# Kernel optimization log

Measured on AMD Instinct MI355X. Metric: run time of the kernel, lower is better.

Reference implementation:

```python
import jax, jax.numpy as jnp
import numpy as np


def _lstm_layer(x, Wih, Whh, b):
    # torch nn.LSTM single layer, batch_first, gates in i,f,g,o order
    B, T, _ = x.shape
    H = Whh.shape[1]
    xg = jnp.einsum('btd,gd->btg', x, Wih) + b  # precompute input gates (B,T,4H)

    def step(carry, g_t):
        h, c = carry
        g = g_t + h @ Whh.T
        i, f, gg, o = jnp.split(g, 4, axis=-1)
        c = jax.nn.sigmoid(f) * c + jax.nn.sigmoid(i) * jnp.tanh(gg)
        h = jax.nn.sigmoid(o) * jnp.tanh(c)
        return (h, c), h

    z = jnp.zeros((B, H), x.dtype)
    _, hs = jax.lax.scan(step, (z, z), jnp.swapaxes(xg, 0, 1))
    return jnp.swapaxes(hs, 0, 1)


def _forward(x, x_lens, word_starts, word_ends, word_lens, tail_frames,
             fW_ih0, fW_hh0, fb0, fW_ih1, fW_hh1, fb1, fW_ih2, fW_hh2, fb2,
             fpW, fpb, wpW, wpb, lnW, lnB, wW_ih, wW_hh, wb, spW, spb):
    B, T, _ = x.shape
    # 3-layer frame LSTM (eval mode: inter-layer dropout disabled)
    h = _lstm_layer(x, fW_ih0, fW_hh0, fb0)
    h = _lstm_layer(h, fW_ih1, fW_hh1, fb1)
    h = _lstm_layer(h, fW_ih2, fW_hh2, fb2)
    # pad_packed_sequence zeros outputs beyond each sequence length
    tmask = (jnp.arange(T)[None, :] < x_lens[:, None]).astype(h.dtype)
    h = h * tmask[..., None]
    y_frame = h @ fpW.T + fpb  # (B,T,srv)

    # ragged per-word tail mean: r_j = mean h[i0:ef], i0 = max(ef-tail, sf)
    W = word_ends.shape[1]
    ef = jnp.minimum(word_ends, x_lens[:, None])
    sf = jnp.maximum(word_starts, 0)
    i0 = jnp.maximum(ef - tail_frames, sf)
    valid = ((jnp.arange(W)[None, :] < word_lens[:, None]) & (word_ends > 0)
             & (ef > sf) & (ef > i0))
    t = jnp.arange(T)
    m = (valid[:, :, None] & (t[None, None, :] >= i0[:, :, None])
         & (t[None, None, :] < ef[:, :, None])).astype(h.dtype)  # (B,W,T)
    cnt = jnp.maximum(m.sum(-1), 1.0)
    reps = jnp.einsum('bwt,bth->bwh', m, h) / cnt[..., None]  # (B,W,FH)

    # word_proj: Linear + LayerNorm + GELU (eval: dropout/noise/word-dropout off)
    r = reps @ wpW.T + wpb
    mu = r.mean(-1, keepdims=True)
    var = ((r - mu) ** 2).mean(-1, keepdims=True)
    r = (r - mu) / jnp.sqrt(var + 1e-5) * lnW + lnB
    r = jax.nn.gelu(r, approximate=False)

    lens = jnp.maximum(word_lens, 1)
    c = _lstm_layer(r, wW_ih, wW_hh, wb)
    wmask = (jnp.arange(W)[None, :] < lens[:, None]).astype(c.dtype)
    c = c * wmask[..., None]  # pad_packed(total_length=W) zeros
    pred_sem = c @ spW.T + spb  # (B,W,srv)
    return y_frame, x_lens, pred_sem


def setup_inputs() -> dict:
    key = jax.random.key(0)
    ks = jax.random.split(key, 24)
    B, T, D, SRV, FH, WR, WH, W = 16, 2000, 80, 512, 512, 256, 256, 100
    x = jax.random.normal(ks[0], (B, T, D), jnp.float32)
    x_lens = jax.random.randint(ks[1], (B,), T // 2, T + 1).at[0].set(T)
    ends = jnp.sort(jax.random.randint(ks[2], (B, W), 1, T + 1), axis=1)
    starts = jnp.concatenate([jnp.zeros((B, 1), ends.dtype), ends[:, :-1]], axis=1)
    word_lens = jax.random.randint(ks[3], (B,), 1, W + 1)

    def u(k, shape, fan):
        s = 1.0 / np.sqrt(fan)
        return jax.random.uniform(k, shape, jnp.float32, -s, s)

    return {
        'x': x, 'x_lens': x_lens, 'word_starts': starts, 'word_ends': ends,
        'word_lens': word_lens, 'tail_frames': 10,
        'fW_ih0': u(ks[4], (4 * FH, D), FH), 'fW_hh0': u(ks[5], (4 * FH, FH), FH), 'fb0': u(ks[6], (4 * FH,), FH),
        'fW_ih1': u(ks[7], (4 * FH, FH), FH), 'fW_hh1': u(ks[8], (4 * FH, FH), FH), 'fb1': u(ks[9], (4 * FH,), FH),
        'fW_ih2': u(ks[10], (4 * FH, FH), FH), 'fW_hh2': u(ks[11], (4 * FH, FH), FH), 'fb2': u(ks[12], (4 * FH,), FH),
        'fpW': u(ks[13], (SRV, FH), FH), 'fpb': u(ks[14], (SRV,), FH),
        'wpW': u(ks[15], (WR, FH), FH), 'wpb': u(ks[16], (WR,), FH),
        'lnW': jnp.ones((WR,), jnp.float32), 'lnB': jnp.zeros((WR,), jnp.float32),
        'wW_ih': u(ks[17], (4 * WH, WR), WH), 'wW_hh': u(ks[18], (4 * WH, WH), WH), 'wb': u(ks[19], (4 * WH,), WH),
        'spW': u(ks[20], (SRV, WH), WH), 'spb': u(ks[21], (SRV,), WH),
    }


def reference(x, x_lens, word_starts, word_ends, word_lens, tail_frames,
              fW_ih0, fW_hh0, fb0, fW_ih1, fW_hh1, fb1, fW_ih2, fW_hh2, fb2,
              fpW, fpb, wpW, wpb, lnW, lnB, wW_ih, wW_hh, wb, spW, spb):
    return _forward(x, x_lens, word_starts, word_ends, word_lens, tail_frames,
                    fW_ih0, fW_hh0, fb0, fW_ih1, fW_hh1, fb1, fW_ih2, fW_hh2, fb2,
                    fpW, fpb, wpW, wpb, lnW, lnB, wW_ih, wW_hh, wb, spW, spb)
```

## Files before the change

kernel.cpp:

```cpp
#include <hip/hip_runtime.h>
#include <math.h>

typedef unsigned short u16;
typedef unsigned int   u32;
typedef unsigned long long u64;
typedef __attribute__((ext_vector_type(8))) short short8;
typedef __attribute__((ext_vector_type(4))) float f32x4;

__device__ __forceinline__ float bf2f(u16 v) { return __uint_as_float(((u32)v) << 16); }
__device__ __forceinline__ u16 f2bf(float f) {
    u32 u = __float_as_uint(f);
    u32 r = (u + 0x7fffu + ((u >> 16) & 1u)) >> 16;
    return (u16)r;
}
__device__ __forceinline__ u32 pk2(float a, float b) {
    return ((u32)f2bf(a)) | (((u32)f2bf(b)) << 16);
}
__device__ __forceinline__ float sigm(float x) { return 1.f / (1.f + __expf(-x)); }
__device__ __forceinline__ f32x4 mfma16(short8 a, short8 b, f32x4 c) {
    return __builtin_amdgcn_mfma_f32_16x16x32_bf16(a, b, c, 0, 0, 0);
}
__device__ __forceinline__ short8 ld8bf(const float* p) {
    short8 r;
#pragma unroll
    for (int j = 0; j < 8; ++j) r[j] = (short)f2bf(p[j]);
    return r;
}
__device__ __forceinline__ short8 ldg16cv(const u16* p) {
    short8 r;
    asm volatile("global_load_dwordx4 %0, %1, off sc0 sc1" : "=v"(r) : "v"(p));
    return r;
}
__device__ __forceinline__ void waitvm() {
    asm volatile("s_waitcnt vmcnt(0)" ::: "memory");
}

#define FLAG_STRIDE 16
#define NPAR 8
#define BIGF (1 << 26)
#define XL_OFF 16384000
#define PS_OFF 16384016

#define WS_FLAGS   0
#define WS_HBUF_F  32768
#define WS_HBUF_W  425984
#define WS_REPS    491520
#define WS_RW      3768320
#define WS_HSEQ    4587520
#define WS_FPWB    6225920

template<int KTIN, bool L0>
__device__ __forceinline__ void frame_body(
    const int layer, const int kwg,
    const float* __restrict__ Wih, const float* __restrict__ Whh, const float* __restrict__ bias,
    const float* __restrict__ x, u16* __restrict__ hbuf, int* __restrict__ flags,
    float* __restrict__ h3out, float* sC, float* scs, u16* sxpad, u16* AsIn, u16* AsOwn)
{
    const int tid  = threadIdx.x;
    const int lane = tid & 63;
    const int wave = tid >> 6;
    const int n16  = lane & 15;
    const int quad = lane >> 4;
    const int koff = quad * 8;

    for (int e = tid; e < 144; e += 128) scs[e] = 0.f;
    if (L0) {
        for (int e = tid; e < 256; e += 128) sxpad[(e >> 4) * 96 + 80 + (e & 15)] = 0;
    }

    const int grow = wave * 1024 + ((n16 >> 3) * 512) + kwg * 8 + (n16 & 7);
    short8 bfr[KTIN + 16];
#pragma unroll
    for (int kt = 0; kt < KTIN; ++kt) {
        short8 v = {0,0,0,0,0,0,0,0};
        const int k = kt * 32 + koff;
        if (L0) { if (k + 8 <= 80) v = ld8bf(Wih + grow * 80 + k); }
        else    { v = ld8bf(Wih + (size_t)grow * 512 + k); }
        bfr[kt] = v;
    }
#pragma unroll
    for (int kt = 0; kt < 16; ++kt)
        bfr[KTIN + kt] = ld8bf(Whh + (size_t)grow * 512 + kt * 32 + koff);

    const int pb = (tid >> 4) & 3;
    const int cb = kwg * 8 + pb * 2;
    const float bI0 = bias[cb],        bI1 = bias[cb + 1];
    const float bF0 = bias[512 + cb],  bF1 = bias[512 + cb + 1];
    const float bG0 = bias[1024 + cb], bG1 = bias[1024 + cb + 1];
    const float bO0 = bias[1536 + cb], bO1 = bias[1536 + cb + 1];

    const int* fP = flags + (layer * 64) * FLAG_STRIDE;
    const int* fO = flags + ((layer + 1) * 64) * FLAG_STRIDE;
    const int* fN = flags + ((layer + 2) * 64) * FLAG_STRIDE;
    int* myflag   = flags + ((layer + 1) * 64 + kwg) * FLAG_STRIDE;
    __syncthreads();

    for (int t = 0; t < 2000; ++t) {
        if (wave == 0) {
            int guard = 0;
            for (;;) {
                const int fp = __hip_atomic_load(fP + lane * FLAG_STRIDE, __ATOMIC_RELAXED, __HIP_MEMORY_SCOPE_AGENT);
                const int fo = __hip_atomic_load(fO + lane * FLAG_STRIDE, __ATOMIC_RELAXED, __HIP_MEMORY_SCOPE_AGENT);
                const int fn = __hip_atomic_load(fN + lane * FLAG_STRIDE, __ATOMIC_RELAXED, __HIP_MEMORY_SCOPE_AGENT);
                if (__all((fp >= t + 1) && (fo >= t) && (fn >= t - 7))) break;
                if (++guard > (1 << 22)) break;
                __builtin_amdgcn_s_sleep(1);
            }
        }
        __syncthreads();

        const u16* hown = hbuf + ((size_t)(layer * NPAR + ((t + 7) & 7))) * 8192;
        short8 rin[8], rown[8];
        float4 xv0, xv1, xv2;
        if (L0) {
            const int e0 = tid, e1 = tid + 128, e2 = tid + 256;
            xv0 = *(const float4*)(x + ((size_t)(e0 / 20) * 2000 + t) * 80 + (e0 % 20) * 4);
            xv1 = *(const float4*)(x + ((size_t)(e1 / 20) * 2000 + t) * 80 + (e1 % 20) * 4);
            if (e2 < 320)
                xv2 = *(const float4*)(x + ((size_t)(e2 / 20) * 2000 + t) * 80 + (e2 % 20) * 4);
        } else {
            const u16* hin = hbuf + ((size_t)((layer - 1) * NPAR + (t & 7))) * 8192;
#pragma unroll
            for (int i = 0; i < 8; ++i) rin[i] = ldg16cv(hin + (tid + 128 * i) * 8);
        }
#pragma unroll
        for (int i = 0; i < 8; ++i) rown[i] = ldg16cv(hown + (tid + 128 * i) * 8);
        waitvm();
        if (L0) {
            const int e0 = tid, e1 = tid + 128, e2 = tid + 256;
            u32* d0 = (u32*)(sxpad + (e0 / 20) * 96 + (e0 % 20) * 4);
            d0[0] = pk2(xv0.x, xv0.y); d0[1] = pk2(xv0.z, xv0.w);
            u32* d1 = (u32*)(sxpad + (e1 / 20) * 96 + (e1 % 20) * 4);
            d1[0] = pk2(xv1.x, xv1.y); d1[1] = pk2(xv1.z, xv1.w);
            if (e2 < 320) {
                u32* d2 = (u32*)(sxpad + (e2 / 20) * 96 + (e2 % 20) * 4);
                d2[0] = pk2(xv2.x, xv2.y); d2[1] = pk2(xv2.z, xv2.w);
            }
        }
#pragma unroll
        for (int i = 0; i < 8; ++i) {
            const int c = tid + 128 * i;
            const int row = c >> 6, col8 = (c & 63) << 3;
            if (!L0) *(short8*)(AsIn + row * 520 + col8) = rin[i];
            *(short8*)(AsOwn + row * 520 + col8) = rown[i];
        }
        __syncthreads();

        f32x4 acc[4] = {{0,0,0,0},{0,0,0,0},{0,0,0,0},{0,0,0,0}};
#pragma unroll
        for (int kt = 0; kt < KTIN; ++kt) {
            short8 a;
            if (L0) a = *(const short8*)(sxpad + n16 * 96 + kt * 32 + koff);
            else    a = *(const short8*)(AsIn + n16 * 520 + kt * 32 + koff);
            acc[kt & 3] = mfma16(a, bfr[kt], acc[kt & 3]);
        }
#pragma unroll
        for (int kt = 0; kt < 16; ++kt) {
            short8 a = *(const short8*)(AsOwn + n16 * 520 + kt * 32 + koff);
            acc[(KTIN + kt) & 3] = mfma16(a, bfr[KTIN + kt], acc[(KTIN + kt) & 3]);
        }
        const f32x4 C = acc[0] + acc[1] + acc[2] + acc[3];
#pragma unroll
        for (int r = 0; r < 4; ++r)
            sC[(wave * 16 + quad * 4 + r) * 17 + n16] = C[r];
        __syncthreads();

        if (tid < 64) {
            const int b = tid & 15, p = tid >> 4;
            u32 pk = 0;
#pragma unroll
            for (int e = 0; e < 2; ++e) {
                const int jl = p * 2 + e;
                const float gi = sC[b * 17 + jl]             + (e ? bI1 : bI0);
                const float gf = sC[b * 17 + 8 + jl]         + (e ? bF1 : bF0);
                const float gg = sC[(16 + b) * 17 + jl]      + (e ? bG1 : bG0);
                const float go = sC[(16 + b) * 17 + 8 + jl]  + (e ? bO1 : bO0);
                const float cp = scs[b * 9 + jl];
                const float cn = sigm(gf) * cp + sigm(gi) * tanhf(gg);
                const float hn = sigm(go) * tanhf(cn);
                scs[b * 9 + jl] = cn;
                pk |= ((u32)f2bf(hn)) << (16 * e);
                if (!L0 && layer == 2)
                    h3out[((size_t)(b * 2000 + t)) * 512 + kwg * 8 + p * 2 + e] = hn;
            }
            u32* hdst = (u32*)(hbuf + ((size_t)(layer * NPAR + (t & 7))) * 8192 + b * 512 + kwg * 8 + p * 2);
            __hip_atomic_store(hdst, pk, __ATOMIC_RELAXED, __HIP_MEMORY_SCOPE_AGENT);
            waitvm();
            if (tid == 0)
                __hip_atomic_store(myflag, t + 1, __ATOMIC_RELAXED, __HIP_MEMORY_SCOPE_AGENT);
        }
    }
}

__global__ __launch_bounds__(128, 1) void k_frame_lstm(
    const float* __restrict__ x,
    const float* __restrict__ Wih0, const float* __restrict__ Whh0, const float* __restrict__ b0,
    const float* __restrict__ Wih1, const float* __restrict__ Whh1, const float* __restrict__ b1,
    const float* __restrict__ Wih2, const float* __restrict__ Whh2, const float* __restrict__ b2,
    u16* hbuf, int* flags, float* h3out)
{
    __shared__ __align__(16) u16 sxpad[16 * 96];
    __shared__ __align__(16) u16 AsIn[16 * 520];
    __shared__ __align__(16) u16 AsOwn[16 * 520];
    __shared__ float sC[32 * 17];
    __shared__ float scs[16 * 9];
    const int wgid = blockIdx.x;
    const int layer = wgid >> 6;
    const int kwg = wgid & 63;
    if (layer == 0)      frame_body<3,  true >(0, kwg, Wih0, Whh0, b0, x, hbuf, flags, h3out, sC, scs, sxpad, AsIn, AsOwn);
    else if (layer == 1) frame_body<16, false>(1, kwg, Wih1, Whh1, b1, x, hbuf, flags, h3out, sC, scs, sxpad, AsIn, AsOwn);
    else                 frame_body<16, false>(2, kwg, Wih2, Whh2, b2, x, hbuf, flags, h3out, sC, scs, sxpad, AsIn, AsOwn);
}

__global__ __launch_bounds__(128, 1) void k_word_lstm(
    const u16* __restrict__ rW, const float* __restrict__ Wih,
    const float* __restrict__ Whh, const float* __restrict__ bias,
    u16* __restrict__ hbufw, int* __restrict__ flags, float* __restrict__ hseq)
{
    __shared__ float sC[32 * 17];
    __shared__ float scs[16 * 9];
    const int tid = threadIdx.x;
    const int lane = tid & 63;
    const int wave = tid >> 6;
    const int n16 = lane & 15;
    const int quad = lane >> 4;
    const int koff = quad * 8;
    const int kwg = blockIdx.x;

    for (int e = tid; e < 144; e += 128) scs[e] = 0.f;
    const int grow = wave * 512 + ((n16 >> 3) * 256) + kwg * 8 + (n16 & 7);
    short8 bfr[16];
#pragma unroll
    for (int kt = 0; kt < 8; ++kt) bfr[kt]     = ld8bf(Wih + (size_t)grow * 256 + kt * 32 + koff);
#pragma unroll
    for (int kt = 0; kt < 8; ++kt) bfr[8 + kt] = ld8bf(Whh + (size_t)grow * 256 + kt * 32 + koff);
    const int pb = (tid >> 4) & 3;
    const int cb = kwg * 8 + pb * 2;
    const float bI0 = bias[cb],       bI1 = bias[cb + 1];
    const float bF0 = bias[256 + cb], bF1 = bias[256 + cb + 1];
    const float bG0 = bias[512 + cb], bG1 = bias[512 + cb + 1];
    const float bO0 = bias[768 + cb], bO1 = bias[768 + cb + 1];
    const int* fO = flags + 320 * FLAG_STRIDE;
    int* myflag   = flags + (320 + kwg) * FLAG_STRIDE;
    __syncthreads();
    const int aoff = n16 * 256 + koff;

    for (int t = 0; t < 100; ++t) {
        if (wave == 0) {
            int guard = 0;
            for (;;) {
                const int fo = (lane < 32)
                    ? __hip_atomic_load(fO + lane * FLAG_STRIDE, __ATOMIC_RELAXED, __HIP_MEMORY_SCOPE_AGENT)
                    : BIGF;
                if (__all(fo >= t)) break;
                if (++guard > (1 << 22)) break;
                __builtin_amdgcn_s_sleep(1);
            }
        }
        __syncthreads();
        const u16* hown = hbufw + ((size_t)((t + 7) & 7)) * 4096;
        short8 ha[8];
#pragma unroll
        for (int kt = 0; kt < 8; ++kt) ha[kt] = ldg16cv(hown + aoff + kt * 32);
        f32x4 acc[4] = {{0,0,0,0},{0,0,0,0},{0,0,0,0},{0,0,0,0}};
#pragma unroll
        for (int kt = 0; kt < 8; ++kt) {
            short8 a = *(const short8*)(rW + ((size_t)(n16 * 100 + t)) * 256 + koff + kt * 32);
            acc[kt & 3] = mfma16(a, bfr[kt], acc[kt & 3]);
        }
        waitvm();
#pragma unroll
        for (int kt = 0; kt < 8; ++kt)
            acc[kt & 3] = mfma16(ha[kt], bfr[8 + kt], acc[kt & 3]);
        const f32x4 C = acc[0] + acc[1] + acc[2] + acc[3];
#pragma unroll
        for (int r = 0; r < 4; ++r) sC[(wave * 16 + quad * 4 + r) * 17 + n16] = C[r];
        __syncthreads();
        if (tid < 64) {
            const int b = tid & 15, p = tid >> 4;
            u32 pk = 0;
#pragma unroll
            for (int e = 0; e < 2; ++e) {
                const int jl = p * 2 + e;
                const float gi = sC[b * 17 + jl]            + (e ? bI1 : bI0);
                const float gf = sC[b * 17 + 8 + jl]        + (e ? bF1 : bF0);
                const float gg = sC[(16 + b) * 17 + jl]     + (e ? bG1 : bG0);
                const float go = sC[(16 + b) * 17 + 8 + jl] + (e ? bO1 : bO0);
                const float cp = scs[b * 9 + jl];
                const float cn = sigm(gf) * cp + sigm(gi) * tanhf(gg);
                const float hn = sigm(go) * tanhf(cn);
                scs[b * 9 + jl] = cn;
                pk |= ((u32)f2bf(hn)) << (16 * e);
                hseq[((size_t)(b * 100 + t)) * 256 + kwg * 8 + p * 2 + e] = hn;
            }
            u32* hdst = (u32*)(hbufw + ((size_t)(t & 7)) * 4096 + b * 256 + kwg * 8 + p * 2);
            __hip_atomic_store(hdst, pk, __ATOMIC_RELAXED, __HIP_MEMORY_SCOPE_AGENT);
            waitvm();
            if (tid == 0)
                __hip_atomic_store(myflag, t + 1, __ATOMIC_RELAXED, __HIP_MEMORY_SCOPE_AGENT);
        }
    }
}

__global__ void k_pool(const float* __restrict__ h3, const int* __restrict__ x_lens,
                       const int* __restrict__ wstarts, const int* __restrict__ wends,
                       const int* __restrict__ wlens, const int* __restrict__ tailp,
                       float* __restrict__ reps)
{
    const int rw = blockIdx.x;
    const int b = rw / 100, w = rw - b * 100;
    const int tid = threadIdx.x;
    const int xl = x_lens[b];
    const int we = wends[rw];
    const int s0 = wstarts[rw];
    const int wl = wlens[b];
    const int tail = tailp[0];
    int ef = we < xl ? we : xl;
    int sf = s0 > 0 ? s0 : 0;
    int i0 = ef - tail; if (i0 < sf) i0 = sf;
    const bool valid = (w < wl) && (we > 0) && (ef > sf) && (ef > i0);
    float a0 = 0.f, a1 = 0.f;
    if (valid) {
        for (int t = i0; t < ef; ++t) {
            const float* hp = h3 + ((size_t)(b * 2000 + t)) * 512;
            a0 += hp[tid];
            a1 += hp[tid + 256];
        }
        const float inv = 1.f / (float)(ef - i0);
        a0 *= inv; a1 *= inv;
    }
    reps[(size_t)rw * 512 + tid] = a0;
    reps[(size_t)rw * 512 + tid + 256] = a1;
}

__global__ __launch_bounds__(256, 2) void k_frame_proj(
    float* __restrict__ y, const int* __restrict__ x_lens,
    const u16* __restrict__ fpWb, const float* __restrict__ fpb)
{
    __shared__ __align__(16) u16 As[16 * 520];
    const int tid = threadIdx.x, lane = tid & 63, wave = tid >> 6;
    const int n16 = lane & 15, quad = lane >> 4, koff = quad * 8;
    const int blk = blockIdx.x;
    const int b = blk / 125;
    const int t0 = (blk - b * 125) * 16;
    const int xl = x_lens[b];
    for (int c = tid; c < 2048; c += 256) {
        const int row = c >> 7;
        const int q = c & 127;
        const int t = t0 + row;
        float4 v = {0.f, 0.f, 0.f, 0.f};
        if (t < xl) v = *(const float4*)(y + ((size_t)(b * 2000 + t)) * 512 + q * 4);
        u32* d = (u32*)(As + row * 520 + q * 4);
        d[0] = pk2(v.x, v.y);
        d[1] = pk2(v.z, v.w);
    }
    __syncthreads();
    const size_t rowbase = (size_t)b * 2000 + t0;
    for (int ct = 0; ct < 8; ++ct) {
        const int col0 = (wave * 8 + ct) * 16;
        f32x4 acc = {0, 0, 0, 0};
#pragma unroll
        for (int kt = 0; kt < 16; ++kt) {
            short8 a = *(const short8*)(As + n16 * 520 + kt * 32 + koff);
            short8 wv = *(const short8*)(fpWb + ((size_t)(col0 + n16)) * 512 + kt * 32 + koff);
            acc = mfma16(a, wv, acc);
        }
        const float bn = fpb[col0 + n16];
#pragma unroll
        for (int r = 0; r < 4; ++r) {
            const int m = quad * 4 + r;
            y[(rowbase + m) * 512 + col0 + n16] = acc[r] + bn;
        }
    }
}

__global__ void k_word_proj(const float* __restrict__ reps, const float* __restrict__ wpW,
                            const float* __restrict__ wpb, const float* __restrict__ lnW,
                            const float* __restrict__ lnB, u16* __restrict__ rW)
{
    __shared__ float sx[512];
    __shared__ float red[512];
    const int tid = threadIdx.x;
    const int row = blockIdx.x;
    for (int k = tid; k < 512; k += 256) sx[k] = reps[(size_t)row * 512 + k];
    __syncthreads();
    float acc = wpb[tid];
    const float4* wr = (const float4*)(wpW + (size_t)tid * 512);
    for (int k4 = 0; k4 < 128; ++k4) {
        const float4 w = wr[k4];
        acc += sx[k4 * 4] * w.x + sx[k4 * 4 + 1] * w.y + sx[k4 * 4 + 2] * w.z + sx[k4 * 4 + 3] * w.w;
    }
    red[tid] = acc; red[256 + tid] = acc * acc;
    __syncthreads();
    for (int s = 128; s > 0; s >>= 1) {
        if (tid < s) { red[tid] += red[tid + s]; red[256 + tid] += red[256 + tid + s]; }
        __syncthreads();
    }
    const float mu = red[0] * (1.f / 256.f);
    float var = red[256] * (1.f / 256.f) - mu * mu;
    if (var < 0.f) var = 0.f;
    const float xn = (acc - mu) * rsqrtf(var + 1e-5f);
    const float yv = xn * lnW[tid] + lnB[tid];
    const float g = 0.5f * yv * (1.0f + erff(yv * 0.70710678118654752f));
    rW[(size_t)row * 256 + tid] = f2bf(g);
}

__global__ void k_pred(const float* __restrict__ hseq, const int* __restrict__ wlens,
                       const float* __restrict__ spW, const float* __restrict__ spb,
                       float* __restrict__ out)
{
    __shared__ float sh[256];
    const int tid = threadIdx.x;
    const int rw = blockIdx.x;
    const int b = rw / 100, w = rw - b * 100;
    int wl = wlens[b]; if (wl < 1) wl = 1;
    const bool valid = (w < wl);
    sh[tid] = valid ? hseq[(size_t)rw * 256 + tid] : 0.f;
    __syncthreads();
    for (int o = tid; o < 512; o += 256) {
        float acc = spb[o];
        const float4* wr = (const float4*)(spW + (size_t)o * 256);
        for (int k4 = 0; k4 < 64; ++k4) {
            const float4 wv = wr[k4];
            acc += sh[k4 * 4] * wv.x + sh[k4 * 4 + 1] * wv.y + sh[k4 * 4 + 2] * wv.z + sh[k4 * 4 + 3] * wv.w;
        }
        out[PS_OFF + (size_t)rw * 512 + o] = acc;
    }
}

__global__ void k_xlens(const int* __restrict__ x_lens, float* __restrict__ out)
{
    const int tid = threadIdx.x;
    if (tid < 16) out[XL_OFF + tid] = (float)x_lens[tid];
}

__global__ void k_cvt(const float* __restrict__ src, u16* __restrict__ dst)
{
    const int e = blockIdx.x * 256 + threadIdx.x;
    const float4 v = *(const float4*)(src + (size_t)e * 4);
    u32* d = (u32*)(dst + (size_t)e * 4);
    d[0] = pk2(v.x, v.y);
    d[1] = pk2(v.z, v.w);
}

__global__ void k_init(u32* __restrict__ p)
{
    const int idx = blockIdx.x * 256 + threadIdx.x;
    u32 v = 0u;
    if (idx < 8192) {
        const int slot = idx >> 4;
        if (slot < 64 || (slot >= 256 && slot < 320)) v = (u32)BIGF;
    }
    p[idx] = v;
}

extern "C" void kernel_launch(void* const* d_in, const int* in_sizes, int n_in,
                              void* d_out, int out_size, void* d_ws, size_t ws_size,
                              hipStream_t stream)
{
    (void)in_sizes; (void)n_in; (void)out_size; (void)ws_size;
    const float* x    = (const float*)d_in[0];
    const int* x_lens = (const int*)d_in[1];
    const int* wstart = (const int*)d_in[2];
    const int* wend   = (const int*)d_in[3];
    const int* wlen   = (const int*)d_in[4];
    const int* tailp  = (const int*)d_in[5];
    const float* Wih0 = (const float*)d_in[6];
    const float* Whh0 = (const float*)d_in[7];
    const float* b0   = (const float*)d_in[8];
    const float* Wih1 = (const float*)d_in[9];
    const float* Whh1 = (const float*)d_in[10];
    const float* b1   = (const float*)d_in[11];
    const float* Wih2 = (const float*)d_in[12];
    const float* Whh2 = (const float*)d_in[13];
    const float* b2   = (const float*)d_in[14];
    const float* fpW  = (const float*)d_in[15];
    const float* fpb  = (const float*)d_in[16];
    const float* wpW  = (const float*)d_in[17];
    const float* wpb  = (const float*)d_in[18];
    const float* lnW  = (const float*)d_in[19];
    const float* lnB  = (const float*)d_in[20];
    const float* wWih = (const float*)d_in[21];
    const float* wWhh = (const float*)d_in[22];
    const float* wb   = (const float*)d_in[23];
    const float* spW  = (const float*)d_in[24];
    const float* spb  = (const float*)d_in[25];

    float* out = (float*)d_out;
    char* ws = (char*)d_ws;
    int* flags  = (int*)(ws + WS_FLAGS);
    u16* hbufF  = (u16*)(ws + WS_HBUF_F);
    u16* hbufW  = (u16*)(ws + WS_HBUF_W);
    float* reps = (float*)(ws + WS_REPS);
    u16* rW     = (u16*)(ws + WS_RW);
    float* hseq = (float*)(ws + WS_HSEQ);
    u16* fpWb   = (u16*)(ws + WS_FPWB);

    k_init<<<480, 256, 0, stream>>>((u32*)d_ws);
    k_cvt<<<256, 256, 0, stream>>>(fpW, fpWb);
    k_frame_lstm<<<192, 128, 0, stream>>>(x, Wih0, Whh0, b0, Wih1, Whh1, b1,
                                          Wih2, Whh2, b2, hbufF, flags, out);
    k_pool<<<1600, 256, 0, stream>>>(out, x_lens, wstart, wend, wlen, tailp, reps);
    k_frame_proj<<<2000, 256, 0, stream>>>(out, x_lens, fpWb, fpb);
    k_word_proj<<<1600, 256, 0, stream>>>(reps, wpW, wpb, lnW, lnB, rW);
    k_word_lstm<<<32, 128, 0, stream>>>(rW, wWih, wWhh, wb, hbufW, flags, hseq);
    k_pred<<<1600, 256, 0, stream>>>(hseq, wlen, spW, spb, out);
    k_xlens<<<1, 64, 0, stream>>>(x_lens, out);
}
```

Before: 7.718 ms.

## Replace per-step flag polling with self-validating bit-inverted hidden-state buffers

Hidden states are now stored bit-inverted, so a zero word means "not yet written". Consumers spin directly on the data until every word is nonzero, which replaces the per-step polling of producer flags. The ring buffer grows to 16 slots, and each workgroup zeroes a slot ahead of use. Only the next layer's progress flag is still checked, which removes a flag round-trip and a barrier from the serial recurrence. The gate nonlinearity now runs on all 128 threads instead of 64, with the cell state kept in registers. The cost is a correctness dependency on the zero-sentinel encoding and on memory ordering between the clearing stores and later writes.

```diff
diff --git a/kernel.cpp b/kernel.cpp
--- a/kernel.cpp
+++ b/kernel.cpp
@@ -6,8 +6,8 @@
 typedef unsigned long long u64;
 typedef __attribute__((ext_vector_type(8))) short short8;
 typedef __attribute__((ext_vector_type(4))) float f32x4;
-
-__device__ __forceinline__ float bf2f(u16 v) { return __uint_as_float(((u32)v) << 16); }
+typedef __attribute__((ext_vector_type(4))) unsigned int u32x4;
+
 __device__ __forceinline__ u16 f2bf(float f) {
     u32 u = __float_as_uint(f);
     u32 r = (u + 0x7fffu + ((u >> 16) & 1u)) >> 16;
@@ -26,35 +26,41 @@
     for (int j = 0; j < 8; ++j) r[j] = (short)f2bf(p[j]);
     return r;
 }
-__device__ __forceinline__ short8 ldg16cv(const u16* p) {
-    short8 r;
+__device__ __forceinline__ u32x4 ldg16cv4(const u16* p) {
+    u32x4 r;
     asm volatile("global_load_dwordx4 %0, %1, off sc0 sc1" : "=v"(r) : "v"(p));
     return r;
 }
 __device__ __forceinline__ void waitvm() {
     asm volatile("s_waitcnt vmcnt(0)" ::: "memory");
 }
+__device__ __forceinline__ void st_not16(u16* dst, u32x4 w) {
+    u32x4 d; d[0] = ~w[0]; d[1] = ~w[1]; d[2] = ~w[2]; d[3] = ~w[3];
+    *(u32x4*)dst = d;
+}
+__device__ __forceinline__ void st_zero16(u16* dst) {
+    u32x4 d = {0u, 0u, 0u, 0u};
+    *(u32x4*)dst = d;
+}
 
 #define FLAG_STRIDE 16
-#define NPAR 8
-#define BIGF (1 << 26)
 #define XL_OFF 16384000
 #define PS_OFF 16384016
 
 #define WS_FLAGS   0
 #define WS_HBUF_F  32768
-#define WS_HBUF_W  425984
-#define WS_REPS    491520
-#define WS_RW      3768320
-#define WS_HSEQ    4587520
-#define WS_FPWB    6225920
-
-template<int KTIN, bool L0>
+#define WS_HBUF_W  819200
+#define WS_REPS    950272
+#define WS_RW      4227072
+#define WS_HSEQ    5046272
+#define WS_FPWB    6684672
+
+template<int KTIN, bool L0, bool HASNEXT>
 __device__ __forceinline__ void frame_body(
     const int layer, const int kwg,
     const float* __restrict__ Wih, const float* __restrict__ Whh, const float* __restrict__ bias,
     const float* __restrict__ x, u16* __restrict__ hbuf, int* __restrict__ flags,
-    float* __restrict__ h3out, float* sC, float* scs, u16* sxpad, u16* AsIn, u16* AsOwn)
+    float* __restrict__ h3out, float* sC, u16* sxpad, u16* AsIn, u16* AsOwn)
 {
     const int tid  = threadIdx.x;
     const int lane = tid & 63;
@@ -63,7 +69,6 @@
     const int quad = lane >> 4;
     const int koff = quad * 8;
 
-    for (int e = tid; e < 144; e += 128) scs[e] = 0.f;
     if (L0) {
         for (int e = tid; e < 256; e += 128) sxpad[(e >> 4) * 96 + 80 + (e & 15)] = 0;
     }
@@ -82,52 +87,63 @@
     for (int kt = 0; kt < 16; ++kt)
         bfr[KTIN + kt] = ld8bf(Whh + (size_t)grow * 512 + kt * 32 + koff);
 
-    const int pb = (tid >> 4) & 3;
-    const int cb = kwg * 8 + pb * 2;
-    const float bI0 = bias[cb],        bI1 = bias[cb + 1];
-    const float bF0 = bias[512 + cb],  bF1 = bias[512 + cb + 1];
-    const float bG0 = bias[1024 + cb], bG1 = bias[1024 + cb + 1];
-    const float bO0 = bias[1536 + cb], bO1 = bias[1536 + cb + 1];
-
-    const int* fP = flags + (layer * 64) * FLAG_STRIDE;
-    const int* fO = flags + ((layer + 1) * 64) * FLAG_STRIDE;
-    const int* fN = flags + ((layer + 2) * 64) * FLAG_STRIDE;
-    int* myflag   = flags + ((layer + 1) * 64 + kwg) * FLAG_STRIDE;
+    const int gb = tid & 15;
+    const int gj = tid >> 4;
+    const int gc = kwg * 8 + gj;
+    const float bI = bias[gc], bF = bias[512 + gc], bG = bias[1024 + gc], bO = bias[1536 + gc];
+    float creg = 0.f;
+
+    int* myflag   = flags + (layer * 64 + kwg) * FLAG_STRIDE;
+    const int* fN = flags + ((layer + 1) * 64) * FLAG_STRIDE;
+    int fnc = 0;
+    u16* lbase = hbuf + (size_t)layer * 16 * 8192;
+    const u16* pbase = hbuf + (size_t)(layer > 0 ? layer - 1 : 0) * 16 * 8192;
     __syncthreads();
 
     for (int t = 0; t < 2000; ++t) {
         if (wave == 0) {
-            int guard = 0;
-            for (;;) {
-                const int fp = __hip_atomic_load(fP + lane * FLAG_STRIDE, __ATOMIC_RELAXED, __HIP_MEMORY_SCOPE_AGENT);
-                const int fo = __hip_atomic_load(fO + lane * FLAG_STRIDE, __ATOMIC_RELAXED, __HIP_MEMORY_SCOPE_AGENT);
-                const int fn = __hip_atomic_load(fN + lane * FLAG_STRIDE, __ATOMIC_RELAXED, __HIP_MEMORY_SCOPE_AGENT);
-                if (__all((fp >= t + 1) && (fo >= t) && (fn >= t - 7))) break;
-                if (++guard > (1 << 22)) break;
-                __builtin_amdgcn_s_sleep(1);
+            if (HASNEXT && !__all(fnc >= t - 6)) {
+                int guard = 0;
+                do {
+                    fnc = __hip_atomic_load(fN + lane * FLAG_STRIDE, __ATOMIC_RELAXED, __HIP_MEMORY_SCOPE_AGENT);
+                    __builtin_amdgcn_s_sleep(1);
+                } while (!__all(fnc >= t - 6) && ++guard < (1 << 22));
             }
-        }
-        __syncthreads();
-
-        const u16* hown = hbuf + ((size_t)(layer * NPAR + ((t + 7) & 7))) * 8192;
-        short8 rin[8], rown[8];
+            u32* z = (u32*)(lbase + ((size_t)((t + 8) & 15)) * 8192)
+                   + (lane & 15) * 256 + kwg * 4 + (lane >> 4);
+            __hip_atomic_store(z, 0u, __ATOMIC_RELAXED, __HIP_MEMORY_SCOPE_AGENT);
+        }
+
         float4 xv0, xv1, xv2;
+        const int e0 = tid, e1 = tid + 128, e2 = tid + 256;
         if (L0) {
-            const int e0 = tid, e1 = tid + 128, e2 = tid + 256;
             xv0 = *(const float4*)(x + ((size_t)(e0 / 20) * 2000 + t) * 80 + (e0 % 20) * 4);
             xv1 = *(const float4*)(x + ((size_t)(e1 / 20) * 2000 + t) * 80 + (e1 % 20) * 4);
             if (e2 < 320)
                 xv2 = *(const float4*)(x + ((size_t)(e2 / 20) * 2000 + t) * 80 + (e2 % 20) * 4);
-        } else {
-            const u16* hin = hbuf + ((size_t)((layer - 1) * NPAR + (t & 7))) * 8192;
-#pragma unroll
-            for (int i = 0; i < 8; ++i) rin[i] = ldg16cv(hin + (tid + 128 * i) * 8);
-        }
-#pragma unroll
-        for (int i = 0; i < 8; ++i) rown[i] = ldg16cv(hown + (tid + 128 * i) * 8);
-        waitvm();
+        }
+
+        u32x4 v[16];
+        const u16* hin  = pbase + ((size_t)(t & 15)) * 8192;
+        const u16* hown = lbase + ((size_t)((t - 1) & 15)) * 8192;
+        u32 pend = (L0 ? 0u : 0x00FFu) | (t > 0 ? 0xFF00u : 0u);
+        int guard = 0;
+        while (pend) {
+#pragma unroll
+            for (int i = 0; i < 8; ++i)
+                if (!L0 && (pend & (1u << i)))   v[i]     = ldg16cv4(hin  + (tid + 128 * i) * 8);
+#pragma unroll
+            for (int i = 0; i < 8; ++i)
+                if (pend & (0x100u << i))        v[8 + i] = ldg16cv4(hown + (tid + 128 * i) * 8);
+            waitvm();
+#pragma unroll
+            for (int i = 0; i < 16; ++i)
+                if ((pend & (1u << i)) && v[i][0] && v[i][1] && v[i][2] && v[i][3])
+                    pend &= ~(1u << i);
+            if (++guard > (1 << 20)) break;
+        }
+
         if (L0) {
-            const int e0 = tid, e1 = tid + 128, e2 = tid + 256;
             u32* d0 = (u32*)(sxpad + (e0 / 20) * 96 + (e0 % 20) * 4);
             d0[0] = pk2(xv0.x, xv0.y); d0[1] = pk2(xv0.z, xv0.w);
             u32* d1 = (u32*)(sxpad + (e1 / 20) * 96 + (e1 % 20) * 4);
@@ -141,8 +157,9 @@
         for (int i = 0; i < 8; ++i) {
             const int c = tid + 128 * i;
             const int row = c >> 6, col8 = (c & 63) << 3;
-            if (!L0) *(short8*)(AsIn + row * 520 + col8) = rin[i];
-            *(short8*)(AsOwn + row * 520 + col8) = rown[i];
+            if (!L0) st_not16(AsIn + row * 520 + col8, v[i]);
+            if (t > 0) st_not16(AsOwn + row * 520 + col8, v[8 + i]);
+            else       st_zero16(AsOwn + row * 520 + col8);
         }
         __syncthreads();
 
@@ -165,30 +182,25 @@
             sC[(wave * 16 + quad * 4 + r) * 17 + n16] = C[r];
         __syncthreads();
 
-        if (tid < 64) {
-            const int b = tid & 15, p = tid >> 4;
-            u32 pk = 0;
-#pragma unroll
-            for (int e = 0; e < 2; ++e) {
-                const int jl = p * 2 + e;
-                const float gi = sC[b * 17 + jl]             + (e ? bI1 : bI0);
-                const float gf = sC[b * 17 + 8 + jl]         + (e ? bF1 : bF0);
-                const float gg = sC[(16 + b) * 17 + jl]      + (e ? bG1 : bG0);
-                const float go = sC[(16 + b) * 17 + 8 + jl]  + (e ? bO1 : bO0);
-                const float cp = scs[b * 9 + jl];
-                const float cn = sigm(gf) * cp + sigm(gi) * tanhf(gg);
-                const float hn = sigm(go) * tanhf(cn);
-                scs[b * 9 + jl] = cn;
-                pk |= ((u32)f2bf(hn)) << (16 * e);
-                if (!L0 && layer == 2)
-                    h3out[((size_t)(b * 2000 + t)) * 512 + kwg * 8 + p * 2 + e] = hn;
-            }
-            u32* hdst = (u32*)(hbuf + ((size_t)(layer * NPAR + (t & 7))) * 8192 + b * 512 + kwg * 8 + p * 2);
-            __hip_atomic_store(hdst, pk, __ATOMIC_RELAXED, __HIP_MEMORY_SCOPE_AGENT);
-            waitvm();
-            if (tid == 0)
-                __hip_atomic_store(myflag, t + 1, __ATOMIC_RELAXED, __HIP_MEMORY_SCOPE_AGENT);
-        }
+        const float gi = sC[gb * 17 + gj]            + bI;
+        const float gf = sC[gb * 17 + 8 + gj]        + bF;
+        const float gg = sC[(16 + gb) * 17 + gj]     + bG;
+        const float go = sC[(16 + gb) * 17 + 8 + gj] + bO;
+        const float cn = sigm(gf) * creg + sigm(gi) * tanhf(gg);
+        const float hn = sigm(go) * tanhf(cn);
+        creg = cn;
+        if (!HASNEXT)
+            h3out[((size_t)(gb * 2000 + t)) * 512 + gc] = hn;
+        const u32 mb = (u32)f2bf(hn);
+        const u32 nb = (u32)__shfl_xor((int)mb, 16, 64);
+        if (!(gj & 1)) {
+            const u32 enc = ~(mb | (nb << 16));
+            u32* hd = (u32*)(lbase + ((size_t)(t & 15)) * 8192)
+                    + gb * 256 + kwg * 4 + (gj >> 1);
+            __hip_atomic_store(hd, enc, __ATOMIC_RELAXED, __HIP_MEMORY_SCOPE_AGENT);
+        }
+        if (tid == 0)
+            __hip_atomic_store(myflag, t + 1, __ATOMIC_RELAXED, __HIP_MEMORY_SCOPE_AGENT);
     }
 }
 
@@ -203,22 +215,20 @@
     __shared__ __align__(16) u16 AsIn[16 * 520];
     __shared__ __align__(16) u16 AsOwn[16 * 520];
     __shared__ float sC[32 * 17];
-    __shared__ float scs[16 * 9];
     const int wgid = blockIdx.x;
     const int layer = wgid >> 6;
     const int kwg = wgid & 63;
-    if (layer == 0)      frame_body<3,  true >(0, kwg, Wih0, Whh0, b0, x, hbuf, flags, h3out, sC, scs, sxpad, AsIn, AsOwn);
-    else if (layer == 1) frame_body<16, false>(1, kwg, Wih1, Whh1, b1, x, hbuf, flags, h3out, sC, scs, sxpad, AsIn, AsOwn);
-    else                 frame_body<16, false>(2, kwg, Wih2, Whh2, b2, x, hbuf, flags, h3out, sC, scs, sxpad, AsIn, AsOwn);
+    if (layer == 0)      frame_body<3,  true,  true >(0, kwg, Wih0, Whh0, b0, x, hbuf, flags, h3out, sC, sxpad, AsIn, AsOwn);
+    else if (layer == 1) frame_body<16, false, true >(1, kwg, Wih1, Whh1, b1, x, hbuf, flags, h3out, sC, sxpad, AsIn, AsOwn);
+    else                 frame_body<16, false, false>(2, kwg, Wih2, Whh2, b2, x, hbuf, flags, h3out, sC, sxpad, AsIn, AsOwn);
 }
 
 __global__ __launch_bounds__(128, 1) void k_word_lstm(
     const u16* __restrict__ rW, const float* __restrict__ Wih,
     const float* __restrict__ Whh, const float* __restrict__ bias,
-    u16* __restrict__ hbufw, int* __restrict__ flags, float* __restrict__ hseq)
+    u16* __restrict__ hbufw, float* __restrict__ hseq)
 {
     __shared__ float sC[32 * 17];
-    __shared__ float scs[16 * 9];
     const int tid = threadIdx.x;
     const int lane = tid & 63;
     const int wave = tid >> 6;
@@ -227,78 +237,75 @@
     const int koff = quad * 8;
     const int kwg = blockIdx.x;
 
-    for (int e = tid; e < 144; e += 128) scs[e] = 0.f;
     const int grow = wave * 512 + ((n16 >> 3) * 256) + kwg * 8 + (n16 & 7);
     short8 bfr[16];
 #pragma unroll
     for (int kt = 0; kt < 8; ++kt) bfr[kt]     = ld8bf(Wih + (size_t)grow * 256 + kt * 32 + koff);
 #pragma unroll
     for (int kt = 0; kt < 8; ++kt) bfr[8 + kt] = ld8bf(Whh + (size_t)grow * 256 + kt * 32 + koff);
-    const int pb = (tid >> 4) & 3;
-    const int cb = kwg * 8 + pb * 2;
-    const float bI0 = bias[cb],       bI1 = bias[cb + 1];
-    const float bF0 = bias[256 + cb], bF1 = bias[256 + cb + 1];
-    const float bG0 = bias[512 + cb], bG1 = bias[512 + cb + 1];
-    const float bO0 = bias[768 + cb], bO1 = bias[768 + cb + 1];
-    const int* fO = flags + 320 * FLAG_STRIDE;
-    int* myflag   = flags + (320 + kwg) * FLAG_STRIDE;
+    const int gb = tid & 15;
+    const int gj = tid >> 4;
+    const int gc = kwg * 8 + gj;
+    const float bI = bias[gc], bF = bias[256 + gc], bG = bias[512 + gc], bO = bias[768 + gc];
+    float creg = 0.f;
     __syncthreads();
     const int aoff = n16 * 256 + koff;
 
     for (int t = 0; t < 100; ++t) {
         if (wave == 0) {
-            int guard = 0;
-            for (;;) {
-                const int fo = (lane < 32)
-                    ? __hip_atomic_load(fO + lane * FLAG_STRIDE, __ATOMIC_RELAXED, __HIP_MEMORY_SCOPE_AGENT)
-                    : BIGF;
-                if (__all(fo >= t)) break;
-                if (++guard > (1 << 22)) break;
-                __builtin_amdgcn_s_sleep(1);
-            }
-        }
-        __syncthreads();
-        const u16* hown = hbufw + ((size_t)((t + 7) & 7)) * 4096;
-        short8 ha[8];
-#pragma unroll
-        for (int kt = 0; kt < 8; ++kt) ha[kt] = ldg16cv(hown + aoff + kt * 32);
+            u32* z = (u32*)(hbufw + ((size_t)((t + 8) & 15)) * 4096)
+                   + (lane & 15) * 128 + kwg * 4 + (lane >> 4);
+            __hip_atomic_store(z, 0u, __ATOMIC_RELAXED, __HIP_MEMORY_SCOPE_AGENT);
+        }
+        u32x4 hv[8];
+        const u16* hown = hbufw + ((size_t)((t - 1) & 15)) * 4096;
+        u32 pend = (t > 0) ? 0xFFu : 0u;
+        int guard = 0;
+        while (pend) {
+#pragma unroll
+            for (int kt = 0; kt < 8; ++kt)
+                if (pend & (1u << kt)) hv[kt] = ldg16cv4(hown + aoff + kt * 32);
+            waitvm();
+#pragma unroll
+            for (int kt = 0; kt < 8; ++kt)
+                if ((pend & (1u << kt)) && hv[kt][0] && hv[kt][1] && hv[kt][2] && hv[kt][3])
+                    pend &= ~(1u << kt);
+            if (++guard > (1 << 20)) break;
+        }
         f32x4 acc[4] = {{0,0,0,0},{0,0,0,0},{0,0,0,0},{0,0,0,0}};
 #pragma unroll
         for (int kt = 0; kt < 8; ++kt) {
             short8 a = *(const short8*)(rW + ((size_t)(n16 * 100 + t)) * 256 + koff + kt * 32);
             acc[kt & 3] = mfma16(a, bfr[kt], acc[kt & 3]);
         }
-        waitvm();
-#pragma unroll
-        for (int kt = 0; kt < 8; ++kt)
-            acc[kt & 3] = mfma16(ha[kt], bfr[8 + kt], acc[kt & 3]);
+        if (t > 0) {
+#pragma unroll
+            for (int kt = 0; kt < 8; ++kt) {
+                u32x4 d; d[0] = ~hv[kt][0]; d[1] = ~hv[kt][1]; d[2] = ~hv[kt][2]; d[3] = ~hv[kt][3];
+                short8 a = __builtin_bit_cast(short8, d);
+                acc[kt & 3] = mfma16(a, bfr[8 + kt], acc[kt & 3]);
+            }
+        }
         const f32x4 C = acc[0] + acc[1] + acc[2] + acc[3];
 #pragma unroll
         for (int r = 0; r < 4; ++r) sC[(wave * 16 + quad * 4 + r) * 17 + n16] = C[r];
         __syncthreads();
-        if (tid < 64) {
-            const int b = tid & 15, p = tid >> 4;
-            u32 pk = 0;
-#pragma unroll
-            for (int e = 0; e < 2; ++e) {
-                const int jl = p * 2 + e;
-                const float gi = sC[b * 17 + jl]            + (e ? bI1 : bI0);
-                const float gf = sC[b * 17 + 8 + jl]        + (e ? bF1 : bF0);
-                const float gg = sC[(16 + b) * 17 + jl]     + (e ? bG1 : bG0);
-                const float go = sC[(16 + b) * 17 + 8 + jl] + (e ? bO1 : bO0);
-                const float cp = scs[b * 9 + jl];
-                const float cn = sigm(gf) * cp + sigm(gi) * tanhf(gg);
-                const float hn = sigm(go) * tanhf(cn);
-                scs[b * 9 + jl] = cn;
-                pk |= ((u32)f2bf(hn)) << (16 * e);
-                hseq[((size_t)(b * 100 + t)) * 256 + kwg * 8 + p * 2 + e] = hn;
-            }
-            u32* hdst = (u32*)(hbufw + ((size_t)(t & 7)) * 4096 + b * 256 + kwg * 8 + p * 2);
-            __hip_atomic_store(hdst, pk, __ATOMIC_RELAXED, __HIP_MEMORY_SCOPE_AGENT);
-            waitvm();
-            if (tid == 0)
-                __hip_atomic_store(myflag, t + 1, __ATOMIC_RELAXED, __HIP_MEMORY_SCOPE_AGENT);
-        }
+
+        const float gi = sC[gb * 17 + gj]            + bI;
+        const float gf = sC[gb * 17 + 8 + gj]        + bF;
+        const float gg = sC[(16 + gb) * 17 + gj]     + bG;
+        const float go = sC[(16 + gb) * 17 + 8 + gj] + bO;
+        const float cn = sigm(gf) * creg + sigm(gi) * tanhf(gg);
+        const float hn = sigm(go) * tanhf(cn);
+        creg = cn;
+        hseq[((size_t)(gb * 100 + t)) * 256 + gc] = hn;
+        const u32 mb = (u32)f2bf(hn);
+        const u32 nb = (u32)__shfl_xor((int)mb, 16, 64);
+        if (!(gj & 1)) {
+            u32* hd = (u32*)(hbufw + ((size_t)(t & 15)) * 4096) + gb * 128 + kwg * 4 + (gj >> 1);
+            __hip_atomic_store(hd, ~(mb | (nb << 16)), __ATOMIC_RELAXED, __HIP_MEMORY_SCOPE_AGENT);
+        }
+        __syncthreads();
     }
 }
 
@@ -445,13 +452,7 @@
 
 __global__ void k_init(u32* __restrict__ p)
 {
-    const int idx = blockIdx.x * 256 + threadIdx.x;
-    u32 v = 0u;
-    if (idx < 8192) {
-        const int slot = idx >> 4;
-        if (slot < 64 || (slot >= 256 && slot < 320)) v = (u32)BIGF;
-    }
-    p[idx] = v;
+    p[blockIdx.x * 256 + threadIdx.x] = 0u;
 }
 
 extern "C" void kernel_launch(void* const* d_in, const int* in_sizes, int n_in,
@@ -496,14 +497,14 @@
     float* hseq = (float*)(ws + WS_HSEQ);
     u16* fpWb   = (u16*)(ws + WS_FPWB);
 
-    k_init<<<480, 256, 0, stream>>>((u32*)d_ws);
+    k_init<<<928, 256, 0, stream>>>((u32*)d_ws);
     k_cvt<<<256, 256, 0, stream>>>(fpW, fpWb);
     k_frame_lstm<<<192, 128, 0, stream>>>(x, Wih0, Whh0, b0, Wih1, Whh1, b1,
                                           Wih2, Whh2, b2, hbufF, flags, out);
     k_pool<<<1600, 256, 0, stream>>>(out, x_lens, wstart, wend, wlen, tailp, reps);
     k_frame_proj<<<2000, 256, 0, stream>>>(out, x_lens, fpWb, fpb);
     k_word_proj<<<1600, 256, 0, stream>>>(reps, wpW, wpb, lnW, lnB, rW);
-    k_word_lstm<<<32, 128, 0, stream>>>(rW, wWih, wWhh, wb, hbufW, flags, hseq);
+    k_word_lstm<<<32, 128, 0, stream>>>(rW, wWih, wWhh, wb, hbufW, hseq);
     k_pred<<<1600, 256, 0, stream>>>(hseq, wlen, spW, spb, out);
     k_xlens<<<1, 64, 0, stream>>>(x_lens, out);
 }
```

Result: slower. 11.28 ms (+46.1%).
